# Performance work log

Measured on AMD Instinct MI355X. Metric: run time of the kernel, lower is better.

The kernel has to match this reference:

```python
import jax, jax.numpy as jnp
import numpy as np

TEMP = 0.1
EPS = 1e-12  # torch F.normalize eps


def _normalize(v):
    return v / jnp.maximum(jnp.linalg.norm(v, axis=1, keepdims=True), EPS)


def _scale_loss(a1, a2, b1, c1):
    # diag of exp(a1 @ a2.T / temp): computed directly from paired rows
    # (same math as eye-mask + row-sum in the original).
    diag = jnp.exp(jnp.sum(a1 * a2, axis=1) / TEMP)            # [B]
    denom = (jnp.exp(a1 @ b1.T / TEMP).sum(1, keepdims=True)
             + jnp.exp(a1 @ c1.T / TEMP).sum(1, keepdims=True))  # [B,1]
    # NOTE: [B] / [B,1] broadcasts to [B,B], exactly as in the torch code.
    return jnp.mean(-jnp.log(diag / denom))


def setup_inputs() -> dict:
    key = jax.random.key(0)
    kx, ky, kz = jax.random.split(key, 3)
    shape = (8192, 128)
    return {
        "x": jax.random.normal(kx, shape, dtype=jnp.float32),
        "y": jax.random.normal(ky, shape, dtype=jnp.float32),
        "z": jax.random.normal(kz, shape, dtype=jnp.float32),
    }


def reference(x, y, z):
    x = _normalize(x)
    y = _normalize(y)
    z = _normalize(z)
    B = x.shape[0] // 2
    x1, x2 = x[:B], x[B:]
    y1, y2 = y[:B], y[B:]
    z1, z2 = z[:B], z[B:]

    loss_scale = (_scale_loss(x1, x2, y1, z1)
                  + _scale_loss(y1, y2, x1, z1)
                  + _scale_loss(z1, z2, x1, y1))

    xyz1 = jnp.concatenate([x1, y1, z1], axis=1)  # [B, 3D]
    xyz2 = jnp.concatenate([x2, y2, z2], axis=1)
    m = jnp.exp(xyz1 @ xyz2.T / TEMP)             # [B, B]
    # [B] / [B,1] -> [B,B] broadcast, matching the torch code.
    loss_view = jnp.mean(-jnp.log(jnp.diagonal(m) / m.sum(1, keepdims=True)))

    return loss_view + loss_scale
```

## Files before the change

### kernel.cpp

```cpp
#include <hip/hip_runtime.h>
#include <hip/hip_bf16.h>

#define BHALF 4096
#define DDIM 128
#define KCAT 384
#define TEMP_INV 10.0f
#define EXP2K 14.426950408889634f
#define PSTRIDE (64 * 4096)

typedef __attribute__((ext_vector_type(8))) short short8;
typedef __attribute__((ext_vector_type(4))) float f32x4;

__device__ __forceinline__ void gload16(const ushort* g, ushort* l) {
  __builtin_amdgcn_global_load_lds(
      (const __attribute__((address_space(1))) unsigned int*)g,
      (__attribute__((address_space(3))) unsigned int*)l, 16, 0, 0);
}

__global__ __launch_bounds__(256) void norm_diag_kernel(
    const float* __restrict__ x, const float* __restrict__ y,
    const float* __restrict__ z, ushort* __restrict__ nrm1,
    ushort* __restrict__ nrm2, float* __restrict__ dxyz) {
  int wave = threadIdx.x >> 6;
  int lane = threadIdx.x & 63;
  int gi = blockIdx.x * 4 + wave;
  int mat = gi >> 12;
  int i = gi & 4095;
  const float* src = (mat == 0 ? x : (mat == 1 ? y : z));
  float2 a = *(const float2*)(src + (size_t)i * DDIM + lane * 2);
  float2 b = *(const float2*)(src + (size_t)(i + BHALF) * DDIM + lane * 2);
  float s1 = a.x * a.x + a.y * a.y;
  float s2 = b.x * b.x + b.y * b.y;
  float d = a.x * b.x + a.y * b.y;
#pragma unroll
  for (int m = 1; m < 64; m <<= 1) {
    s1 += __shfl_xor(s1, m, 64);
    s2 += __shfl_xor(s2, m, 64);
    d += __shfl_xor(d, m, 64);
  }
  float r1 = 1.0f / fmaxf(sqrtf(s1), 1e-12f);
  float r2 = 1.0f / fmaxf(sqrtf(s2), 1e-12f);
  ushort* d1 = nrm1 + (size_t)i * KCAT + mat * DDIM + lane * 2;
  ushort* d2 = nrm2 + (size_t)i * KCAT + mat * DDIM + lane * 2;
  __hip_bfloat162 o1, o2;
  o1.x = __float2bfloat16(a.x * r1);
  o1.y = __float2bfloat16(a.y * r1);
  o2.x = __float2bfloat16(b.x * r2);
  o2.y = __float2bfloat16(b.y * r2);
  *(__hip_bfloat162*)d1 = o1;
  *(__hip_bfloat162*)d2 = o2;
  if (lane == 0) dxyz[mat * BHALF + i] = d * r1 * r2;
}


__device__ __forceinline__ void flush_cheap(f32x4 (&acc)[4][4],
                                            float* __restrict__ dst, int base,
                                            int lane) {
#pragma unroll
  for (int m = 0; m < 4; ++m) {
    float s = 0.0f;
#pragma unroll
    for (int n = 0; n < 4; ++n)
#pragma unroll
      for (int r = 0; r < 4; ++r) s += exp2f(acc[m][n][r] * EXP2K);
    s += __shfl_xor(s, 16, 64);
    s += __shfl_xor(s, 32, 64);
    if (lane < 16) dst[base + m * 16 + lane] = s;
  }
}

__device__ __forceinline__ void flush_full(f32x4 (&acc)[4][4],
                                           float* __restrict__ rs,
                                           float* __restrict__ cs, int rbase,
                                           int cbase, int lane) {
#pragma unroll
  for (int m = 0; m < 4; ++m)
#pragma unroll
    for (int n = 0; n < 4; ++n)
#pragma unroll
      for (int r = 0; r < 4; ++r)
        acc[m][n][r] = exp2f(acc[m][n][r] * EXP2K);

#pragma unroll
  for (int m = 0; m < 4; ++m) {
    float rsum[4];
#pragma unroll
    for (int r = 0; r < 4; ++r)
      rsum[r] = acc[m][0][r] + acc[m][1][r] + acc[m][2][r] + acc[m][3][r];
#pragma unroll
    for (int r = 0; r < 4; ++r) {
      rsum[r] += __shfl_xor(rsum[r], 1, 64);
      rsum[r] += __shfl_xor(rsum[r], 2, 64);
      rsum[r] += __shfl_xor(rsum[r], 4, 64);
      rsum[r] += __shfl_xor(rsum[r], 8, 64);
    }
    if ((lane & 15) == 0) {
      int rb = rbase + m * 16 + (lane >> 4) * 4;
#pragma unroll
      for (int r = 0; r < 4; ++r) rs[rb + r] = rsum[r];
    }
  }

#pragma unroll
  for (int n = 0; n < 4; ++n) {
    float csum = 0.0f;
#pragma unroll
    for (int m = 0; m < 4; ++m)
#pragma unroll
      for (int r = 0; r < 4; ++r) csum += acc[m][n][r];
    csum += __shfl_xor(csum, 16, 64);
    csum += __shfl_xor(csum, 32, 64);
    if (lane < 16) cs[cbase + n * 16 + lane] = csum;
  }
}

__global__ __launch_bounds__(256) void gram_slab_kernel(
    const ushort* __restrict__ nrm1, const ushort* __restrict__ nrm2,
    float* __restrict__ parts) {
  __shared__ ushort As[4][128][32];
  __shared__ ushort Bs[4][128][32];

  int tid = threadIdx.x;
  int lane = tid & 63;
  int wave = tid >> 6;
  int wr = wave >> 1;
  int wc = wave & 1;
  int g = (blockIdx.z == 0) ? 3 : (int)blockIdx.z - 1;
  int fid = (int)blockIdx.x + 32 * (int)blockIdx.y;
  int swz = (fid & 7) * 128 + (fid >> 3);
  int bi = swz & 31;
  int bj = swz >> 5;
  int rowbase = bi * 128;
  int colbase = bj * 128;

  const ushort* Ab;
  const ushort* Bb;
  int nslab;
  float* rs;
  float* cs;
  int rslot = (bj * 2 + wc) * 4096;
  int cslot = (bi * 2 + wr) * 4096;
  if (g == 3) {
    Ab = nrm1;       Bb = nrm2;       nslab = 3;
    rs = parts + 6 * PSTRIDE + rslot; cs = nullptr;
  } else if (g == 0) {
    Ab = nrm1;       Bb = nrm1 + 128; nslab = 1;
    rs = parts + 0 * PSTRIDE + rslot; cs = parts + 1 * PSTRIDE + cslot;
  } else if (g == 1) {
    Ab = nrm1;       Bb = nrm1 + 256; nslab = 1;
    rs = parts + 2 * PSTRIDE + rslot; cs = parts + 3 * PSTRIDE + cslot;
  } else {
    Ab = nrm1 + 128; Bb = nrm1 + 256; nslab = 1;
    rs = parts + 4 * PSTRIDE + rslot; cs = parts + 5 * PSTRIDE + cslot;
  }

  int srow = lane >> 2;
  int schunk = ((lane & 3) ^ ((lane >> 3) & 3)) << 3;
  const ushort* gA =
      Ab + (size_t)(rowbase + wave * 32 + srow) * KCAT + schunk;
  const ushort* gB =
      Bb + (size_t)(colbase + wave * 32 + srow) * KCAT + schunk;

  int rsel = lane & 15;
  int slot8 = (((lane >> 4) ^ ((rsel >> 1) & 3)) << 3);

  f32x4 acc[4][4] = {};

  for (int slab = 0; slab < nslab; ++slab) {
    if (slab) {
      __builtin_amdgcn_s_barrier();
      __builtin_amdgcn_sched_barrier(0);
    }
    int k0 = slab * 128;
#pragma unroll
    for (int s = 0; s < 4; ++s) {
#pragma unroll
      for (int rg = 0; rg < 2; ++rg) {
        gload16(gA + k0 + s * 32 + (size_t)rg * 16 * KCAT,
                &As[s][wave * 32 + rg * 16][0]);
        gload16(gB + k0 + s * 32 + (size_t)rg * 16 * KCAT,
                &Bs[s][wave * 32 + rg * 16][0]);
      }
    }
    asm volatile("s_waitcnt vmcnt(0)" ::: "memory");
    __builtin_amdgcn_s_barrier();
    __builtin_amdgcn_sched_barrier(0);

    if (g == 3) {
#pragma unroll
      for (int kk = 0; kk < 4; ++kk) {
        short8 af[4], bf[4];
#pragma unroll
        for (int m = 0; m < 4; ++m)
          af[m] = *(const short8*)&As[kk][wr * 64 + m * 16 + rsel][slot8];
#pragma unroll
        for (int n = 0; n < 4; ++n)
          bf[n] = *(const short8*)&Bs[kk][wc * 64 + n * 16 + rsel][slot8];
#pragma unroll
        for (int m = 0; m < 4; ++m)
#pragma unroll
          for (int n = 0; n < 4; ++n)
            acc[m][n] = __builtin_amdgcn_mfma_f32_16x16x32_bf16(
                bf[n], af[m], acc[m][n], 0, 0, 0);
      }
    } else {
#pragma unroll
      for (int kk = 0; kk < 4; ++kk) {
        short8 af[4], bf[4];
#pragma unroll
        for (int m = 0; m < 4; ++m)
          af[m] = *(const short8*)&As[kk][wr * 64 + m * 16 + rsel][slot8];
#pragma unroll
        for (int n = 0; n < 4; ++n)
          bf[n] = *(const short8*)&Bs[kk][wc * 64 + n * 16 + rsel][slot8];
#pragma unroll
        for (int m = 0; m < 4; ++m)
#pragma unroll
          for (int n = 0; n < 4; ++n)
            acc[m][n] = __builtin_amdgcn_mfma_f32_16x16x32_bf16(
                af[m], bf[n], acc[m][n], 0, 0, 0);
      }
    }
  }

  if (g == 3)
    flush_cheap(acc, rs, rowbase + wr * 64, lane);
  else
    flush_full(acc, rs, cs, rowbase + wr * 64, colbase + wc * 64, lane);
}

__global__ __launch_bounds__(256) void reduce_parts_kernel(
    const float* __restrict__ parts, float* __restrict__ sums7) {
  int f = blockIdx.x * 256 + threadIdx.x;
  int a = f >> 12;
  int i = f & 4095;
  const float* p = parts + (size_t)a * PSTRIDE + i;
  float s = 0.0f;
#pragma unroll 8
  for (int slot = 0; slot < 64; ++slot) s += p[slot * 4096];
  sums7[f] = s;
}

__global__ __launch_bounds__(256) void loss_kernel(
    const float* __restrict__ s7, const float* __restrict__ dxyz,
    float* __restrict__ out) {
  int tid = threadIdx.x;
  float acc = 0.0f;
  for (int i = tid; i < BHALF; i += 256) {
    float rs0 = s7[i];
    float cs0 = s7[4096 + i];
    float rs1 = s7[2 * 4096 + i];
    float cs1 = s7[3 * 4096 + i];
    float rs2 = s7[4 * 4096 + i];
    float cs2 = s7[5 * 4096 + i];
    float rs3 = s7[6 * 4096 + i];
    float dxv = dxyz[i];
    float dyv = dxyz[4096 + i];
    float dzv = dxyz[2 * 4096 + i];
    float lx = logf(rs0 + rs1) - TEMP_INV * dxv;
    float ly = logf(cs0 + rs2) - TEMP_INV * dyv;
    float lz = logf(cs1 + cs2) - TEMP_INV * dzv;
    float lv = logf(rs3) - TEMP_INV * (dxv + dyv + dzv);
    acc += lx + ly + lz + lv;
  }
  __shared__ float red[4];
#pragma unroll
  for (int m = 1; m < 64; m <<= 1) acc += __shfl_xor(acc, m, 64);
  if ((tid & 63) == 0) red[tid >> 6] = acc;
  __syncthreads();
  if (tid == 0)
    out[0] = (red[0] + red[1] + red[2] + red[3]) * (1.0f / 4096.0f);
}

extern "C" void kernel_launch(void* const* d_in, const int* in_sizes, int n_in,
                              void* d_out, int out_size, void* d_ws,
                              size_t ws_size, hipStream_t stream) {
  const float* x = (const float*)d_in[0];
  const float* y = (const float*)d_in[1];
  const float* z = (const float*)d_in[2];
  char* ws = (char*)d_ws;
  ushort* nrm1 = (ushort*)ws;
  ushort* nrm2 = nrm1 + (size_t)BHALF * KCAT;
  float* parts = (float*)(ws + 2 * (size_t)BHALF * KCAT * sizeof(ushort));
  float* dxyz = parts + 7 * PSTRIDE;
  float* sums7 = dxyz + 3 * 4096;

  norm_diag_kernel<<<3 * BHALF / 4, 256, 0, stream>>>(x, y, z, nrm1, nrm2,
                                                      dxyz);
  gram_slab_kernel<<<dim3(32, 32, 4), 256, 0, stream>>>(nrm1, nrm2, parts);
  reduce_parts_kernel<<<112, 256, 0, stream>>>(parts, sums7);
  loss_kernel<<<1, 256, 0, stream>>>(sums7, dxyz, (float*)d_out);
}
```

Measured before the change: 74.72 us.

## Split gram tile across eight waves with smaller per-wave accumulator

The gram kernel now runs 512 threads per block (8 waves as a 4x2 grid), each wave owning a 32x64 sub-tile instead of 64x64, which halves accumulator registers and splits the global-to-LDS loads across more waves. Column partial sums now come from four row-waves per tile, so the parts buffer is re-laid out with 128 column slots and the reduce and loss kernels are updated to match. The aim is more latency hiding and more MFMA issue parallelism per CU. The cost is more redundant B-fragment LDS reads per block and a larger partial-sum buffer to reduce.

```diff
diff --git a/kernel.cpp b/kernel.cpp
--- a/kernel.cpp
+++ b/kernel.cpp
@@ -6,7 +6,15 @@
 #define KCAT 384
 #define TEMP_INV 10.0f
 #define EXP2K 14.426950408889634f
-#define PSTRIDE (64 * 4096)
+
+#define OFF_RS0 0
+#define OFF_RS1 (64 * 4096)
+#define OFF_RS2 (128 * 4096)
+#define OFF_RS3 (192 * 4096)
+#define OFF_CS0 (256 * 4096)
+#define OFF_CS1 (384 * 4096)
+#define OFF_CS2 (512 * 4096)
+#define PARTS_TOTAL (640 * 4096)
 
 typedef __attribute__((ext_vector_type(8))) short short8;
 typedef __attribute__((ext_vector_type(4))) float f32x4;
@@ -53,11 +61,11 @@
 }
 
 
-__device__ __forceinline__ void flush_cheap(f32x4 (&acc)[4][4],
-                                            float* __restrict__ dst, int base,
-                                            int lane) {
-#pragma unroll
-  for (int m = 0; m < 4; ++m) {
+__device__ __forceinline__ void flush_cheap8(f32x4 (&acc)[2][4],
+                                             float* __restrict__ dst,
+                                             int base, int lane) {
+#pragma unroll
+  for (int m = 0; m < 2; ++m) {
     float s = 0.0f;
 #pragma unroll
     for (int n = 0; n < 4; ++n)
@@ -69,12 +77,12 @@
   }
 }
 
-__device__ __forceinline__ void flush_full(f32x4 (&acc)[4][4],
-                                           float* __restrict__ rs,
-                                           float* __restrict__ cs, int rbase,
-                                           int cbase, int lane) {
-#pragma unroll
-  for (int m = 0; m < 4; ++m)
+__device__ __forceinline__ void flush_full8(f32x4 (&acc)[2][4],
+                                            float* __restrict__ rs,
+                                            float* __restrict__ cs, int rbase,
+                                            int cbase, int lane) {
+#pragma unroll
+  for (int m = 0; m < 2; ++m)
 #pragma unroll
     for (int n = 0; n < 4; ++n)
 #pragma unroll
@@ -82,7 +90,7 @@
         acc[m][n][r] = exp2f(acc[m][n][r] * EXP2K);
 
 #pragma unroll
-  for (int m = 0; m < 4; ++m) {
+  for (int m = 0; m < 2; ++m) {
     float rsum[4];
 #pragma unroll
     for (int r = 0; r < 4; ++r)
@@ -105,7 +113,7 @@
   for (int n = 0; n < 4; ++n) {
     float csum = 0.0f;
 #pragma unroll
-    for (int m = 0; m < 4; ++m)
+    for (int m = 0; m < 2; ++m)
 #pragma unroll
       for (int r = 0; r < 4; ++r) csum += acc[m][n][r];
     csum += __shfl_xor(csum, 16, 64);
@@ -114,7 +122,7 @@
   }
 }
 
-__global__ __launch_bounds__(256) void gram_slab_kernel(
+__global__ __launch_bounds__(512) void gram_slab_kernel(
     const ushort* __restrict__ nrm1, const ushort* __restrict__ nrm2,
     float* __restrict__ parts) {
   __shared__ ushort As[4][128][32];
@@ -139,32 +147,32 @@
   float* rs;
   float* cs;
   int rslot = (bj * 2 + wc) * 4096;
-  int cslot = (bi * 2 + wr) * 4096;
+  int cslot = (bi * 4 + wr) * 4096;
   if (g == 3) {
     Ab = nrm1;       Bb = nrm2;       nslab = 3;
-    rs = parts + 6 * PSTRIDE + rslot; cs = nullptr;
+    rs = parts + OFF_RS3 + rslot; cs = nullptr;
   } else if (g == 0) {
     Ab = nrm1;       Bb = nrm1 + 128; nslab = 1;
-    rs = parts + 0 * PSTRIDE + rslot; cs = parts + 1 * PSTRIDE + cslot;
+    rs = parts + OFF_RS0 + rslot; cs = parts + OFF_CS0 + cslot;
   } else if (g == 1) {
     Ab = nrm1;       Bb = nrm1 + 256; nslab = 1;
-    rs = parts + 2 * PSTRIDE + rslot; cs = parts + 3 * PSTRIDE + cslot;
+    rs = parts + OFF_RS1 + rslot; cs = parts + OFF_CS1 + cslot;
   } else {
     Ab = nrm1 + 128; Bb = nrm1 + 256; nslab = 1;
-    rs = parts + 4 * PSTRIDE + rslot; cs = parts + 5 * PSTRIDE + cslot;
+    rs = parts + OFF_RS2 + rslot; cs = parts + OFF_CS2 + cslot;
   }
 
   int srow = lane >> 2;
   int schunk = ((lane & 3) ^ ((lane >> 3) & 3)) << 3;
   const ushort* gA =
-      Ab + (size_t)(rowbase + wave * 32 + srow) * KCAT + schunk;
+      Ab + (size_t)(rowbase + wave * 16 + srow) * KCAT + schunk;
   const ushort* gB =
-      Bb + (size_t)(colbase + wave * 32 + srow) * KCAT + schunk;
+      Bb + (size_t)(colbase + wave * 16 + srow) * KCAT + schunk;
 
   int rsel = lane & 15;
   int slot8 = (((lane >> 4) ^ ((rsel >> 1) & 3)) << 3);
 
-  f32x4 acc[4][4] = {};
+  f32x4 acc[2][4] = {};
 
   for (int slab = 0; slab < nslab; ++slab) {
     if (slab) {
@@ -174,13 +182,8 @@
     int k0 = slab * 128;
 #pragma unroll
     for (int s = 0; s < 4; ++s) {
-#pragma unroll
-      for (int rg = 0; rg < 2; ++rg) {
-        gload16(gA + k0 + s * 32 + (size_t)rg * 16 * KCAT,
-                &As[s][wave * 32 + rg * 16][0]);
-        gload16(gB + k0 + s * 32 + (size_t)rg * 16 * KCAT,
-                &Bs[s][wave * 32 + rg * 16][0]);
-      }
+      gload16(gA + k0 + s * 32, &As[s][wave * 16][0]);
+      gload16(gB + k0 + s * 32, &Bs[s][wave * 16][0]);
     }
     asm volatile("s_waitcnt vmcnt(0)" ::: "memory");
     __builtin_amdgcn_s_barrier();
@@ -189,15 +192,15 @@
     if (g == 3) {
 #pragma unroll
       for (int kk = 0; kk < 4; ++kk) {
-        short8 af[4], bf[4];
-#pragma unroll
-        for (int m = 0; m < 4; ++m)
-          af[m] = *(const short8*)&As[kk][wr * 64 + m * 16 + rsel][slot8];
+        short8 af[2], bf[4];
+#pragma unroll
+        for (int m = 0; m < 2; ++m)
+          af[m] = *(const short8*)&As[kk][wr * 32 + m * 16 + rsel][slot8];
 #pragma unroll
         for (int n = 0; n < 4; ++n)
           bf[n] = *(const short8*)&Bs[kk][wc * 64 + n * 16 + rsel][slot8];
 #pragma unroll
-        for (int m = 0; m < 4; ++m)
+        for (int m = 0; m < 2; ++m)
 #pragma unroll
           for (int n = 0; n < 4; ++n)
             acc[m][n] = __builtin_amdgcn_mfma_f32_16x16x32_bf16(
@@ -206,15 +209,15 @@
     } else {
 #pragma unroll
       for (int kk = 0; kk < 4; ++kk) {
-        short8 af[4], bf[4];
-#pragma unroll
-        for (int m = 0; m < 4; ++m)
-          af[m] = *(const short8*)&As[kk][wr * 64 + m * 16 + rsel][slot8];
+        short8 af[2], bf[4];
+#pragma unroll
+        for (int m = 0; m < 2; ++m)
+          af[m] = *(const short8*)&As[kk][wr * 32 + m * 16 + rsel][slot8];
 #pragma unroll
         for (int n = 0; n < 4; ++n)
           bf[n] = *(const short8*)&Bs[kk][wc * 64 + n * 16 + rsel][slot8];
 #pragma unroll
-        for (int m = 0; m < 4; ++m)
+        for (int m = 0; m < 2; ++m)
 #pragma unroll
           for (int n = 0; n < 4; ++n)
             acc[m][n] = __builtin_amdgcn_mfma_f32_16x16x32_bf16(
@@ -224,9 +227,9 @@
   }
 
   if (g == 3)
-    flush_cheap(acc, rs, rowbase + wr * 64, lane);
+    flush_cheap8(acc, rs, rowbase + wr * 32, lane);
   else
-    flush_full(acc, rs, cs, rowbase + wr * 64, colbase + wc * 64, lane);
+    flush_full8(acc, rs, cs, rowbase + wr * 32, colbase + wc * 64, lane);
 }
 
 __global__ __launch_bounds__(256) void reduce_parts_kernel(
@@ -234,10 +237,11 @@
   int f = blockIdx.x * 256 + threadIdx.x;
   int a = f >> 12;
   int i = f & 4095;
-  const float* p = parts + (size_t)a * PSTRIDE + i;
+  int off = (a < 4) ? a * 64 : 256 + (a - 4) * 128;
+  int cnt = (a < 4) ? 64 : 128;
+  const float* p = parts + (size_t)off * 4096 + i;
   float s = 0.0f;
-#pragma unroll 8
-  for (int slot = 0; slot < 64; ++slot) s += p[slot * 4096];
+  for (int slot = 0; slot < cnt; ++slot) s += p[(size_t)slot * 4096];
   sums7[f] = s;
 }
 
@@ -248,12 +252,12 @@
   float acc = 0.0f;
   for (int i = tid; i < BHALF; i += 256) {
     float rs0 = s7[i];
-    float cs0 = s7[4096 + i];
-    float rs1 = s7[2 * 4096 + i];
-    float cs1 = s7[3 * 4096 + i];
-    float rs2 = s7[4 * 4096 + i];
-    float cs2 = s7[5 * 4096 + i];
-    float rs3 = s7[6 * 4096 + i];
+    float rs1 = s7[4096 + i];
+    float rs2 = s7[2 * 4096 + i];
+    float rs3 = s7[3 * 4096 + i];
+    float cs0 = s7[4 * 4096 + i];
+    float cs1 = s7[5 * 4096 + i];
+    float cs2 = s7[6 * 4096 + i];
     float dxv = dxyz[i];
     float dyv = dxyz[4096 + i];
     float dzv = dxyz[2 * 4096 + i];
@@ -282,12 +286,12 @@
   ushort* nrm1 = (ushort*)ws;
   ushort* nrm2 = nrm1 + (size_t)BHALF * KCAT;
   float* parts = (float*)(ws + 2 * (size_t)BHALF * KCAT * sizeof(ushort));
-  float* dxyz = parts + 7 * PSTRIDE;
+  float* dxyz = parts + PARTS_TOTAL;
   float* sums7 = dxyz + 3 * 4096;
 
   norm_diag_kernel<<<3 * BHALF / 4, 256, 0, stream>>>(x, y, z, nrm1, nrm2,
                                                       dxyz);
-  gram_slab_kernel<<<dim3(32, 32, 4), 256, 0, stream>>>(nrm1, nrm2, parts);
+  gram_slab_kernel<<<dim3(32, 32, 4), 512, 0, stream>>>(nrm1, nrm2, parts);
   reduce_parts_kernel<<<112, 256, 0, stream>>>(parts, sums7);
   loss_kernel<<<1, 256, 0, stream>>>(sums7, dxyz, (float*)d_out);
 }
```

Result: slower. 102.7 us (+37.5%).
